# Kernel optimization log

Hardware: AMD Instinct MI355X
Metric: run time of the kernel (lower is better)

Reference implementation:

```python
import jax, jax.numpy as jnp
import numpy as np

B, C, P, H, W, K = 8, 64, 64, 256, 256, 3
BN_EPS = 1e-5


def setup_inputs() -> dict:
    key = jax.random.key(0)
    k0, k1, k2, k3 = jax.random.split(key, 4)
    x = jax.random.normal(k0, (B, C, H, W), dtype=jnp.float32)
    dw_w = jax.random.normal(k1, (C, K, K), dtype=jnp.float32) * (1.0 / K)
    pw_w = jax.random.normal(k2, (P, C), dtype=jnp.float32) * (1.0 / np.sqrt(C))
    gamma = jnp.ones((P,), dtype=jnp.float32)
    beta = jnp.zeros((P,), dtype=jnp.float32)
    mean = jnp.zeros((P,), dtype=jnp.float32)
    var = jnp.ones((P,), dtype=jnp.float32)
    conv_w = jax.random.normal(k3, (1, P), dtype=jnp.float32) * (1.0 / np.sqrt(P))
    return dict(x=x, dw_w=dw_w, pw_w=pw_w, gamma=gamma, beta=beta,
                mean=mean, var=var, conv_w=conv_w)


def reference(x, dw_w, pw_w, gamma, beta, mean, var, conv_w):
    # Faithful to the torch forward: x[:, i:] = relu6(dw_conv[i](x[:, i:i+1]))
    # broadcasts each 1-channel result over channels i..C-1, so iteration i
    # consumes iteration i-1's output -> a sequential chain seeded by x[:, 0].
    def step(y, w):  # y: [B, H, W], w: [K, K]
        o = jax.lax.conv_general_dilated(
            y[:, None, :, :], w[None, None, :, :],
            window_strides=(1, 1), padding='SAME')[:, 0]
        o = jnp.clip(o, 0.0, 6.0)  # ReLU6
        return o, o

    _, ys = jax.lax.scan(step, x[:, 0], dw_w)      # [C, B, H, W]

    # pointwise conv (1x1, no bias)
    h = jnp.einsum('pc,cbhw->bphw', pw_w, ys)       # [B, P, H, W]

    # BatchNorm (inference form with running stats) + ReLU6
    scale = gamma * jax.lax.rsqrt(var + BN_EPS)
    h = h * scale[None, :, None, None] + (beta - mean * scale)[None, :, None, None]
    h = jnp.clip(h, 0.0, 6.0)

    # final 1x1 conv P -> 1 (no bias)
    out = jnp.einsum('op,bphw->bohw', conv_w, h)    # [B, 1, H, W]
    return out
```

## Files before the change

kernel.cpp:

```cpp
#include <hip/hip_runtime.h>
#include <hip/hip_bf16.h>

#define B_    8
#define C_    64
#define P_    64
#define H_    256
#define W_    256
#define BHW_  (B_ * H_ * W_)
#define BN_EPS 1e-5f

#define CHUNK 16
#define SWC   64

__device__ __forceinline__ float dpp_row_shr1(float v) {
    return __int_as_float(__builtin_amdgcn_update_dpp(
        0, __float_as_int(v), 0x111, 0xF, 0xF, true));
}
__device__ __forceinline__ float dpp_row_shl1(float v) {
    return __int_as_float(__builtin_amdgcn_update_dpp(
        0, __float_as_int(v), 0x101, 0xF, 0xF, true));
}

__device__ __forceinline__ short f2bf(float x) {
    unsigned u = __float_as_uint(x);
    unsigned r = (u + 0x7FFFu + ((u >> 16) & 1u)) >> 16;
    return (short)r;
}
__device__ __forceinline__ float bf2f(short h) {
    return __uint_as_float(((unsigned)(unsigned short)h) << 16);
}

typedef __attribute__((ext_vector_type(8))) short bf16x8;
typedef __attribute__((ext_vector_type(4))) float f32x4;

__global__ __launch_bounds__(1024, 8) void chain_kernel(
    const float* __restrict__ src,
    size_t src_batch_stride,
    const float* __restrict__ dw,
    float* __restrict__ ys,
    int c0)
{
    __shared__ __align__(16) float buf0[66 * SWC];
    __shared__ __align__(16) float buf1[66 * SWC];

    const int tid = threadIdx.x;
    const int row = tid >> 4;
    const int seg = tid & 15;
    const int lx  = seg * 4;
    const int b   = blockIdx.z;
    const int ty0 = blockIdx.y * 32;
    const int tx0 = blockIdx.x * 32;
    const int gy  = ty0 - 16 + row;
    const int gx  = tx0 - 16 + lx;
    const bool inImg = (gy >= 0) && (gy < H_) && (gx >= 0) && (gx < W_);
    const float msk = inImg ? 1.0f : 0.0f;

    float4 v = make_float4(0.f, 0.f, 0.f, 0.f);
    if (inImg)
        v = *(const float4*)(src + (size_t)b * src_batch_stride
                             + (size_t)gy * W_ + gx);

    float* cur = buf0;
    float* nxt = buf1;
    const int cell = (row + 1) * SWC + lx;
    *(float4*)&cur[cell] = v;
    if (row == 0) {
        float4 z = make_float4(0.f, 0.f, 0.f, 0.f);
        *(float4*)&buf0[lx] = z;  *(float4*)&buf0[65 * SWC + lx] = z;
        *(float4*)&buf1[lx] = z;  *(float4*)&buf1[65 * SWC + lx] = z;
    }
    __syncthreads();

    const bool wOK = (row >= 16) && (row < 48) && (seg >= 4) && (seg < 12);
    float* gbase = ys + (size_t)c0 * BHW_ + ((size_t)b * H_ + gy) * W_ + gx;

#pragma unroll
    for (int i = 0; i < CHUNK; ++i) {
        const float w0 = dw[i*9+0], w1 = dw[i*9+1], w2 = dw[i*9+2];
        const float w3 = dw[i*9+3], w4 = dw[i*9+4], w5 = dw[i*9+5];
        const float w6 = dw[i*9+6], w7 = dw[i*9+7], w8 = dw[i*9+8];

        float4 rT = *(const float4*)&cur[cell - SWC];
        float4 rM = *(const float4*)&cur[cell];
        float4 rB = *(const float4*)&cur[cell + SWC];

        float tl = dpp_row_shr1(rT.w), tr = dpp_row_shl1(rT.x);
        float ml = dpp_row_shr1(rM.w), mr = dpp_row_shl1(rM.x);
        float bl = dpp_row_shr1(rB.w), br = dpp_row_shl1(rB.x);

        float s0 = fmaf(tl,   w0, fmaf(rT.x, w1, fmaf(rT.y, w2,
                   fmaf(ml,   w3, fmaf(rM.x, w4, fmaf(rM.y, w5,
                   fmaf(bl,   w6, fmaf(rB.x, w7, rB.y * w8))))))));
        float s1 = fmaf(rT.x, w0, fmaf(rT.y, w1, fmaf(rT.z, w2,
                   fmaf(rM.x, w3, fmaf(rM.y, w4, fmaf(rM.z, w5,
                   fmaf(rB.x, w6, fmaf(rB.y, w7, rB.z * w8))))))));
        float s2 = fmaf(rT.y, w0, fmaf(rT.z, w1, fmaf(rT.w, w2,
                   fmaf(rM.y, w3, fmaf(rM.z, w4, fmaf(rM.w, w5,
                   fmaf(rB.y, w6, fmaf(rB.z, w7, rB.w * w8))))))));
        float s3 = fmaf(rT.z, w0, fmaf(rT.w, w1, fmaf(tr,   w2,
                   fmaf(rM.z, w3, fmaf(rM.w, w4, fmaf(mr,   w5,
                   fmaf(rB.z, w6, fmaf(rB.w, w7, br   * w8))))))));
        float4 ov;
        ov.x = fminf(fmaxf(s0, 0.f), 6.f) * msk;
        ov.y = fminf(fmaxf(s1, 0.f), 6.f) * msk;
        ov.z = fminf(fmaxf(s2, 0.f), 6.f) * msk;
        ov.w = fminf(fmaxf(s3, 0.f), 6.f) * msk;

        if (i < CHUNK - 1) {
            *(float4*)&nxt[cell] = ov;
            __syncthreads();
            float* tmp = cur; cur = nxt; nxt = tmp;
        }
        if (wOK)
            *(float4*)(gbase + (size_t)i * BHW_) = ov;
    }
}

__global__ __launch_bounds__(256) void fuse_mfma(
    const float* __restrict__ ys,
    const float* __restrict__ pw_w,
    const float* __restrict__ gamma,
    const float* __restrict__ beta,
    const float* __restrict__ mean,
    const float* __restrict__ var,
    const float* __restrict__ conv_w,
    float* __restrict__ out)
{
    __shared__ short yh[64 * 88];
    __shared__ short yl[64 * 88];
    __shared__ float2 bc[P_];

    const int tid  = threadIdx.x;
    const int lane = tid & 63;
    const int wv   = tid >> 6;
    const int nIdx = lane & 15;
    const int quad = lane >> 4;

    if (tid < P_) {
        float sc = gamma[tid] * rsqrtf(var[tid] + BN_EPS);
        bc[tid] = make_float2(beta[tid] - mean[tid] * sc, conv_w[tid]);
    }

    bf16x8 Ah[4][2], Al[4][2];
#pragma unroll
    for (int pt = 0; pt < 4; ++pt) {
        const int p = pt * 16 + nIdx;
        const float sc = gamma[p] * rsqrtf(var[p] + BN_EPS);
#pragma unroll
        for (int kt = 0; kt < 2; ++kt) {
            const float* ap = pw_w + p * C_ + kt * 32 + quad * 8;
            bf16x8 hh, ll;
#pragma unroll
            for (int j = 0; j < 8; ++j) {
                float a = ap[j] * sc;
                short h = f2bf(a);
                hh[j] = h;
                ll[j] = f2bf(a - bf2f(h));
            }
            Ah[pt][kt] = hh;
            Al[pt][kt] = ll;
        }
    }
    __syncthreads();

    const int px_ = tid & 63;
    const int c0_ = (tid >> 6) * 16;

    for (int tile = blockIdx.x; tile < BHW_ / 64; tile += gridDim.x) {
        const size_t base = (size_t)tile * 64;

        float yv[16];
#pragma unroll
        for (int j = 0; j < 16; ++j)
            yv[j] = ys[(size_t)(c0_ + j) * BHW_ + base + px_];

        __syncthreads();

        short hs[16], ls[16];
#pragma unroll
        for (int j = 0; j < 16; ++j) {
            short h = f2bf(yv[j]);
            hs[j] = h;
            ls[j] = f2bf(yv[j] - bf2f(h));
        }
        *(bf16x8*)&yh[px_ * 88 + c0_]     = *(bf16x8*)&hs[0];
        *(bf16x8*)&yh[px_ * 88 + c0_ + 8] = *(bf16x8*)&hs[8];
        *(bf16x8*)&yl[px_ * 88 + c0_]     = *(bf16x8*)&ls[0];
        *(bf16x8*)&yl[px_ * 88 + c0_ + 8] = *(bf16x8*)&ls[8];

        __syncthreads();

        f32x4 acc[4];
#pragma unroll
        for (int pt = 0; pt < 4; ++pt) acc[pt] = (f32x4){0.f, 0.f, 0.f, 0.f};

        const int col = wv * 16 + nIdx;
#pragma unroll
        for (int kt = 0; kt < 2; ++kt) {
            bf16x8 Bh = *(bf16x8*)&yh[col * 88 + kt * 32 + quad * 8];
            bf16x8 Bl = *(bf16x8*)&yl[col * 88 + kt * 32 + quad * 8];
#pragma unroll
            for (int pt = 0; pt < 4; ++pt) {
                acc[pt] = __builtin_amdgcn_mfma_f32_16x16x32_bf16(
                    Ah[pt][kt], Bh, acc[pt], 0, 0, 0);
                acc[pt] = __builtin_amdgcn_mfma_f32_16x16x32_bf16(
                    Ah[pt][kt], Bl, acc[pt], 0, 0, 0);
                acc[pt] = __builtin_amdgcn_mfma_f32_16x16x32_bf16(
                    Al[pt][kt], Bh, acc[pt], 0, 0, 0);
            }
        }

        float sum = 0.f;
#pragma unroll
        for (int pt = 0; pt < 4; ++pt) {
#pragma unroll
            for (int r = 0; r < 4; ++r) {
                const int p = pt * 16 + quad * 4 + r;
                float2 b = bc[p];
                float v = fminf(fmaxf(acc[pt][r] + b.x, 0.f), 6.f);
                sum = fmaf(b.y, v, sum);
            }
        }
        sum += __shfl_xor(sum, 16, 64);
        sum += __shfl_xor(sum, 32, 64);
        if (lane < 16)
            out[base + wv * 16 + lane] = sum;
    }
}

extern "C" void kernel_launch(void* const* d_in, const int* in_sizes, int n_in,
                              void* d_out, int out_size, void* d_ws, size_t ws_size,
                              hipStream_t stream) {
    const float* x      = (const float*)d_in[0];
    const float* dw_w   = (const float*)d_in[1];
    const float* pw_w   = (const float*)d_in[2];
    const float* gamma  = (const float*)d_in[3];
    const float* beta   = (const float*)d_in[4];
    const float* mean   = (const float*)d_in[5];
    const float* var    = (const float*)d_in[6];
    const float* conv_w = (const float*)d_in[7];
    float* out = (float*)d_out;

    float* ys = (float*)d_ws;

    dim3 cgrid(W_ / 32, H_ / 32, B_);

    chain_kernel<<<cgrid, 1024, 0, stream>>>(
        x, (size_t)C_ * H_ * W_, dw_w, ys, 0);
    for (int k = 1; k < C_ / CHUNK; ++k) {
        int c0 = k * CHUNK;
        chain_kernel<<<cgrid, 1024, 0, stream>>>(
            ys + (size_t)(c0 - 1) * BHW_, (size_t)H_ * W_,
            dw_w + c0 * 9, ys, c0);
    }

    fuse_mfma<<<1024, 256, 0, stream>>>(
        ys, pw_w, gamma, beta, mean, var, conv_w, out);
}
```

Before: 273.8 us.

## Store chain activations as fp16, replace block barriers with per-wave flags

Intermediate ys activations are now written as fp16 instead of fp32, which halves the workspace write and read traffic. A separate fp32 seed buffer keeps the chain's boundary exactly between launches. The pointwise MFMA kernel uses fp16 MFMAs with a hi/lo split of the weights only, so each tile needs 2 MFMAs instead of 3. The per-iteration __syncthreads is replaced by neighbour-wave progress flags in shared memory that are polled with spin-waits, which relaxes global synchronization. The trade-off is fp16 rounding of activations in the range 0–6, and a possible correctness or deadlock risk from the flag-based inter-wave sync, which has no release/acquire guarantee across buffer reuse.

After: 270.8 us. About the same (-1.1%).

```diff
diff --git a/kernel.cpp b/kernel.cpp
--- a/kernel.cpp
+++ b/kernel.cpp
@@ -12,6 +12,11 @@
 #define CHUNK 16
 #define SWC   64
 
+typedef _Float16 half4v __attribute__((ext_vector_type(4)));
+typedef _Float16 half8v __attribute__((ext_vector_type(8)));
+typedef _Float16 half2v __attribute__((ext_vector_type(2)));
+typedef __attribute__((ext_vector_type(4))) float f32x4;
+
 __device__ __forceinline__ float dpp_row_shr1(float v) {
     return __int_as_float(__builtin_amdgcn_update_dpp(
         0, __float_as_int(v), 0x111, 0xF, 0xF, true));
@@ -20,50 +25,41 @@
     return __int_as_float(__builtin_amdgcn_update_dpp(
         0, __float_as_int(v), 0x101, 0xF, 0xF, true));
 }
-
-__device__ __forceinline__ short f2bf(float x) {
-    unsigned u = __float_as_uint(x);
-    unsigned r = (u + 0x7FFFu + ((u >> 16) & 1u)) >> 16;
-    return (short)r;
-}
-__device__ __forceinline__ float bf2f(short h) {
-    return __uint_as_float(((unsigned)(unsigned short)h) << 16);
-}
-
-typedef __attribute__((ext_vector_type(8))) short bf16x8;
-typedef __attribute__((ext_vector_type(4))) float f32x4;
 
 __global__ __launch_bounds__(1024, 8) void chain_kernel(
     const float* __restrict__ src,
     size_t src_batch_stride,
     const float* __restrict__ dw,
-    float* __restrict__ ys,
+    _Float16* __restrict__ ysh,
+    float* __restrict__ seed_out,
     int c0)
 {
     __shared__ __align__(16) float buf0[66 * SWC];
     __shared__ __align__(16) float buf1[66 * SWC];
-
-    const int tid = threadIdx.x;
-    const int row = tid >> 4;
-    const int seg = tid & 15;
-    const int lx  = seg * 4;
-    const int b   = blockIdx.z;
-    const int ty0 = blockIdx.y * 32;
-    const int tx0 = blockIdx.x * 32;
-    const int gy  = ty0 - 16 + row;
-    const int gx  = tx0 - 16 + lx;
+    __shared__ int prog[16];
+
+    const int tid  = threadIdx.x;
+    const int w    = tid >> 6;
+    const int lane = tid & 63;
+    const int row  = tid >> 4;
+    const int seg  = tid & 15;
+    const int lx   = seg * 4;
+    const int b    = blockIdx.z;
+    const int ty0  = blockIdx.y * 32;
+    const int tx0  = blockIdx.x * 32;
+    const int gy   = ty0 - 16 + row;
+    const int gx   = tx0 - 16 + lx;
     const bool inImg = (gy >= 0) && (gy < H_) && (gx >= 0) && (gx < W_);
     const float msk = inImg ? 1.0f : 0.0f;
+    const int cell = (row + 1) * SWC + lx;
+
+    if (tid < 16) prog[tid] = 0;
 
     float4 v = make_float4(0.f, 0.f, 0.f, 0.f);
     if (inImg)
         v = *(const float4*)(src + (size_t)b * src_batch_stride
                              + (size_t)gy * W_ + gx);
-
-    float* cur = buf0;
-    float* nxt = buf1;
-    const int cell = (row + 1) * SWC + lx;
-    *(float4*)&cur[cell] = v;
+    *(float4*)&buf0[cell] = v;
     if (row == 0) {
         float4 z = make_float4(0.f, 0.f, 0.f, 0.f);
         *(float4*)&buf0[lx] = z;  *(float4*)&buf0[65 * SWC + lx] = z;
@@ -71,14 +67,25 @@
     }
     __syncthreads();
 
+    volatile int* vp = prog;
+    const int wm1 = (w == 0)  ? 0  : w - 1;
+    const int wp1 = (w == 15) ? 15 : w + 1;
+
     const bool wOK = (row >= 16) && (row < 48) && (seg >= 4) && (seg < 12);
-    float* gbase = ys + (size_t)c0 * BHW_ + ((size_t)b * H_ + gy) * W_ + gx;
+    const size_t goff = (size_t)(b * H_ + gy) * W_ + gx;
+    _Float16* gb = ysh + (size_t)c0 * BHW_ + (wOK ? goff : 0);
+    float* sb = seed_out ? seed_out + (wOK ? goff : 0) : nullptr;
 
 #pragma unroll
     for (int i = 0; i < CHUNK; ++i) {
         const float w0 = dw[i*9+0], w1 = dw[i*9+1], w2 = dw[i*9+2];
         const float w3 = dw[i*9+3], w4 = dw[i*9+4], w5 = dw[i*9+5];
         const float w6 = dw[i*9+6], w7 = dw[i*9+7], w8 = dw[i*9+8];
+
+        while (vp[wm1] < i || vp[wp1] < i) {  }
+
+        float* cur = (i & 1) ? buf1 : buf0;
+        float* nxt = (i & 1) ? buf0 : buf1;
 
         float4 rT = *(const float4*)&cur[cell - SWC];
         float4 rM = *(const float4*)&cur[cell];
@@ -108,16 +115,23 @@
 
         if (i < CHUNK - 1) {
             *(float4*)&nxt[cell] = ov;
-            __syncthreads();
-            float* tmp = cur; cur = nxt; nxt = tmp;
-        }
-        if (wOK)
-            *(float4*)(gbase + (size_t)i * BHW_) = ov;
+            __threadfence_block();
+            if (lane == 0) vp[w] = i + 1;
+        }
+
+        if (wOK) {
+            half4v hv;
+            hv.x = (_Float16)ov.x; hv.y = (_Float16)ov.y;
+            hv.z = (_Float16)ov.z; hv.w = (_Float16)ov.w;
+            *(half4v*)(gb + (size_t)i * BHW_) = hv;
+            if (i == CHUNK - 1 && sb)
+                *(float4*)sb = ov;
+        }
     }
 }
 
 __global__ __launch_bounds__(256) void fuse_mfma(
-    const float* __restrict__ ys,
+    const _Float16* __restrict__ ysh,
     const float* __restrict__ pw_w,
     const float* __restrict__ gamma,
     const float* __restrict__ beta,
@@ -126,8 +140,7 @@
     const float* __restrict__ conv_w,
     float* __restrict__ out)
 {
-    __shared__ short yh[64 * 88];
-    __shared__ short yl[64 * 88];
+    __shared__ _Float16 yt[64 * 88];
     __shared__ float2 bc[P_];
 
     const int tid  = threadIdx.x;
@@ -141,7 +154,7 @@
         bc[tid] = make_float2(beta[tid] - mean[tid] * sc, conv_w[tid]);
     }
 
-    bf16x8 Ah[4][2], Al[4][2];
+    half8v Ah[4][2], Al[4][2];
 #pragma unroll
     for (int pt = 0; pt < 4; ++pt) {
         const int p = pt * 16 + nIdx;
@@ -149,13 +162,13 @@
 #pragma unroll
         for (int kt = 0; kt < 2; ++kt) {
             const float* ap = pw_w + p * C_ + kt * 32 + quad * 8;
-            bf16x8 hh, ll;
+            half8v hh, ll;
 #pragma unroll
             for (int j = 0; j < 8; ++j) {
                 float a = ap[j] * sc;
-                short h = f2bf(a);
+                _Float16 h = (_Float16)a;
                 hh[j] = h;
-                ll[j] = f2bf(a - bf2f(h));
+                ll[j] = (_Float16)(a - (float)h);
             }
             Ah[pt][kt] = hh;
             Al[pt][kt] = ll;
@@ -163,30 +176,24 @@
     }
     __syncthreads();
 
-    const int px_ = tid & 63;
-    const int c0_ = (tid >> 6) * 16;
+    const int px2 = (tid & 31) * 2;
+    const int c8  = (tid >> 5) * 8;
 
     for (int tile = blockIdx.x; tile < BHW_ / 64; tile += gridDim.x) {
         const size_t base = (size_t)tile * 64;
 
-        float yv[16];
-#pragma unroll
-        for (int j = 0; j < 16; ++j)
-            yv[j] = ys[(size_t)(c0_ + j) * BHW_ + base + px_];
+        half2v yv[8];
+#pragma unroll
+        for (int j = 0; j < 8; ++j)
+            yv[j] = *(const half2v*)(ysh + (size_t)(c8 + j) * BHW_ + base + px2);
 
         __syncthreads();
 
-        short hs[16], ls[16];
-#pragma unroll
-        for (int j = 0; j < 16; ++j) {
-            short h = f2bf(yv[j]);
-            hs[j] = h;
-            ls[j] = f2bf(yv[j] - bf2f(h));
-        }
-        *(bf16x8*)&yh[px_ * 88 + c0_]     = *(bf16x8*)&hs[0];
-        *(bf16x8*)&yh[px_ * 88 + c0_ + 8] = *(bf16x8*)&hs[8];
-        *(bf16x8*)&yl[px_ * 88 + c0_]     = *(bf16x8*)&ls[0];
-        *(bf16x8*)&yl[px_ * 88 + c0_ + 8] = *(bf16x8*)&ls[8];
+        half8v e0, e1;
+#pragma unroll
+        for (int j = 0; j < 8; ++j) { e0[j] = yv[j].x; e1[j] = yv[j].y; }
+        *(half8v*)&yt[px2 * 88 + c8]       = e0;
+        *(half8v*)&yt[(px2 + 1) * 88 + c8] = e1;
 
         __syncthreads();
 
@@ -197,16 +204,13 @@
         const int col = wv * 16 + nIdx;
 #pragma unroll
         for (int kt = 0; kt < 2; ++kt) {
-            bf16x8 Bh = *(bf16x8*)&yh[col * 88 + kt * 32 + quad * 8];
-            bf16x8 Bl = *(bf16x8*)&yl[col * 88 + kt * 32 + quad * 8];
+            half8v Bv = *(half8v*)&yt[col * 88 + kt * 32 + quad * 8];
 #pragma unroll
             for (int pt = 0; pt < 4; ++pt) {
-                acc[pt] = __builtin_amdgcn_mfma_f32_16x16x32_bf16(
-                    Ah[pt][kt], Bh, acc[pt], 0, 0, 0);
-                acc[pt] = __builtin_amdgcn_mfma_f32_16x16x32_bf16(
-                    Ah[pt][kt], Bl, acc[pt], 0, 0, 0);
-                acc[pt] = __builtin_amdgcn_mfma_f32_16x16x32_bf16(
-                    Al[pt][kt], Bh, acc[pt], 0, 0, 0);
+                acc[pt] = __builtin_amdgcn_mfma_f32_16x16x32_f16(
+                    Ah[pt][kt], Bv, acc[pt], 0, 0, 0);
+                acc[pt] = __builtin_amdgcn_mfma_f32_16x16x32_f16(
+                    Al[pt][kt], Bv, acc[pt], 0, 0, 0);
             }
         }
 
@@ -216,9 +220,9 @@
 #pragma unroll
             for (int r = 0; r < 4; ++r) {
                 const int p = pt * 16 + quad * 4 + r;
-                float2 b = bc[p];
-                float v = fminf(fmaxf(acc[pt][r] + b.x, 0.f), 6.f);
-                sum = fmaf(b.y, v, sum);
+                float2 bcv = bc[p];
+                float vv = fminf(fmaxf(acc[pt][r] + bcv.x, 0.f), 6.f);
+                sum = fmaf(bcv.y, vv, sum);
             }
         }
         sum += __shfl_xor(sum, 16, 64);
@@ -241,19 +245,20 @@
     const float* conv_w = (const float*)d_in[7];
     float* out = (float*)d_out;
 
-    float* ys = (float*)d_ws;
+    _Float16* ysh = (_Float16*)d_ws;
+    float* seeds = (float*)((char*)d_ws + (size_t)C_ * BHW_ * sizeof(_Float16));
 
     dim3 cgrid(W_ / 32, H_ / 32, B_);
 
     chain_kernel<<<cgrid, 1024, 0, stream>>>(
-        x, (size_t)C_ * H_ * W_, dw_w, ys, 0);
+        x, (size_t)C_ * H_ * W_, dw_w, ysh, seeds, 0);
     for (int k = 1; k < C_ / CHUNK; ++k) {
-        int c0 = k * CHUNK;
+        float* seed_out = (k < 3) ? seeds + (size_t)k * BHW_ : nullptr;
         chain_kernel<<<cgrid, 1024, 0, stream>>>(
-            ys + (size_t)(c0 - 1) * BHW_, (size_t)H_ * W_,
-            dw_w + c0 * 9, ys, c0);
+            seeds + (size_t)(k - 1) * BHW_, (size_t)H_ * W_,
+            dw_w + k * CHUNK * 9, ysh, seed_out, k * CHUNK);
     }
 
     fuse_mfma<<<1024, 256, 0, stream>>>(
-        ys, pw_w, gamma, beta, mean, var, conv_w, out);
-}
+        ysh, pw_w, gamma, beta, mean, var, conv_w, out);
+}
```
